# Kernel tuning notes

Hardware: AMD Instinct MI355X
Metric: run time of the kernel (lower is better)

## Reference

```python
import jax, jax.numpy as jnp
import numpy as np

# LeViT AttentionSubsample (use_conv=False), BatchNorm folded in eval mode (running stats).
B, RES, STRIDE, RES_OUT = 512, 14, 2, 7
N, NQ = RES * RES, RES_OUT * RES_OUT          # 196, 49
C, H, KD, VD = 256, 8, 16, 32                 # in_dim, heads, key_dim, val_dim
KV_DIM, Q_DIM, V_ATTN, OUT_DIM = H * (KD + VD), H * KD, H * VD, 384
EPS = 1e-5
SCALE = KD ** -0.5


def _bias_idxs():
    ii, jj = np.meshgrid(np.arange(RES), np.arange(RES), indexing='ij')
    k_pos = np.stack([ii.ravel(), jj.ravel()])                      # [2, 196]
    qi, qj = np.meshgrid(np.arange(0, RES, STRIDE), np.arange(0, RES, STRIDE), indexing='ij')
    q_pos = np.stack([qi.ravel(), qj.ravel()])                      # [2, 49]
    rel = np.abs(q_pos[:, :, None] - k_pos[:, None, :])             # [2, 49, 196]
    return jnp.asarray(rel[0] * RES + rel[1], dtype=jnp.int32)      # [49, 196]


def setup_inputs() -> dict:
    key = jax.random.key(0)
    ks = jax.random.split(key, 8)
    f32 = jnp.float32
    inp = {
        'x': jax.random.normal(ks[0], (B, N, C), f32),
        # LinearNorm kv: Linear(C -> KV_DIM, no bias) + BN1d
        'W_kv': jax.random.normal(ks[1], (KV_DIM, C), f32) * 0.05,
        'g_kv': jnp.ones((KV_DIM,), f32), 'b_kv': jnp.zeros((KV_DIM,), f32),
        'm_kv': jax.random.normal(ks[2], (KV_DIM,), f32) * 0.02,
        'v_kv': jax.random.uniform(ks[3], (KV_DIM,), f32) + 0.5,
        # LinearNorm q (after subsample)
        'W_q': jax.random.normal(ks[4], (Q_DIM, C), f32) * 0.05,
        'g_q': jnp.ones((Q_DIM,), f32), 'b_q': jnp.zeros((Q_DIM,), f32),
        'm_q': jax.random.normal(ks[5], (Q_DIM,), f32) * 0.02,
        'v_q': jax.random.uniform(ks[5], (Q_DIM,), f32) + 0.5,
        # proj: hardswish + LinearNorm(V_ATTN -> OUT_DIM)
        'W_proj': jax.random.normal(ks[6], (OUT_DIM, V_ATTN), f32) * 0.05,
        'g_proj': jnp.ones((OUT_DIM,), f32), 'b_proj': jnp.zeros((OUT_DIM,), f32),
        'm_proj': jax.random.normal(ks[7], (OUT_DIM,), f32) * 0.02,
        'v_proj': jax.random.uniform(ks[7], (OUT_DIM,), f32) + 0.5,
        'attention_biases': jax.random.normal(ks[2], (H, N), f32) * 0.02,
        'bias_idxs': _bias_idxs(),
    }
    return inp


def _linear_norm(x, W, g, b, m, v):
    y = jnp.einsum('...i,oi->...o', x, W)
    return (y - m) * (g * jax.lax.rsqrt(v + EPS)) + b


def _hardswish(x):
    return x * jnp.clip(x + 3.0, 0.0, 6.0) * (1.0 / 6.0)


def reference(x, W_kv, g_kv, b_kv, m_kv, v_kv, W_q, g_q, b_q, m_q, v_q,
              W_proj, g_proj, b_proj, m_proj, v_proj, attention_biases, bias_idxs):
    Bx = x.shape[0]
    kv = _linear_norm(x, W_kv, g_kv, b_kv, m_kv, v_kv).reshape(Bx, N, H, KD + VD)
    k, v = kv[..., :KD], kv[..., KD:]                                # [B,N,H,KD],[B,N,H,VD]
    xq = x.reshape(Bx, RES, RES, C)[:, ::STRIDE, ::STRIDE].reshape(Bx, NQ, C)
    q = _linear_norm(xq, W_q, g_q, b_q, m_q, v_q).reshape(Bx, NQ, H, KD)
    bias = attention_biases[:, bias_idxs]                            # [H, NQ, N]
    attn = jnp.einsum('bqhd,bkhd->bhqk', q, k) * SCALE + bias        # [B,H,NQ,N]
    attn = jax.nn.softmax(attn, axis=-1)
    o = jnp.einsum('bhqk,bkhd->bqhd', attn, v).reshape(Bx, NQ, V_ATTN)
    return _linear_norm(_hardswish(o), W_proj, g_proj, b_proj, m_proj, v_proj)
```

## Files before the change

kernel.cpp:

```cpp
#include <hip/hip_runtime.h>


#define Bn   512
#define Nn   196
#define NQn  49
#define Cn   256
#define Hn   8

typedef float    float4v __attribute__((ext_vector_type(4)));
typedef _Float16 half8v  __attribute__((ext_vector_type(8)));
typedef _Float16 half4v  __attribute__((ext_vector_type(4)));

__global__ __launch_bounds__(256) void prep_kernel(
    const float* __restrict__ Wkv, const float* __restrict__ Wq,
    const float* __restrict__ Wp,
    const float* __restrict__ g_kv, const float* __restrict__ b_kv,
    const float* __restrict__ m_kv, const float* __restrict__ v_kv,
    const float* __restrict__ g_q,  const float* __restrict__ b_q,
    const float* __restrict__ m_q,  const float* __restrict__ v_q,
    const float* __restrict__ g_p,  const float* __restrict__ b_p,
    const float* __restrict__ m_p,  const float* __restrict__ v_p,
    const float* __restrict__ ab,   const int* __restrict__ idxs,
    _Float16* __restrict__ WkvF, _Float16* __restrict__ WqF,
    _Float16* __restrict__ WpF,
    float* __restrict__ kv_s, float* __restrict__ kv_sh,
    float* __restrict__ q_s,  float* __restrict__ q_sh,
    float* __restrict__ p_s,  float* __restrict__ p_sh,
    float* __restrict__ biasF)
{
  int i = blockIdx.x * 256 + threadIdx.x;
  if (i < 12288) {
    int lane = i & 63, kc = (i >> 6) & 7, tile = i >> 9;
    const float* src = Wkv + (size_t)(tile * 16 + (lane & 15)) * Cn + kc * 32 + (lane >> 4) * 8;
    half8v hv;
#pragma unroll
    for (int j = 0; j < 8; ++j) hv[j] = (_Float16)src[j];
    *reinterpret_cast<half8v*>(WkvF + (size_t)i * 8) = hv;
    return;
  }
  i -= 12288;
  if (i < 4096) {
    int lane = i & 63, kc = (i >> 6) & 7, tile = i >> 9;
    const float* src = Wq + (size_t)(tile * 16 + (lane & 15)) * Cn + kc * 32 + (lane >> 4) * 8;
    half8v hv;
#pragma unroll
    for (int j = 0; j < 8; ++j) hv[j] = (_Float16)src[j];
    *reinterpret_cast<half8v*>(WqF + (size_t)i * 8) = hv;
    return;
  }
  i -= 4096;
  if (i < 12288) {
    int lane = i & 63, kc = (i >> 6) & 7, tile = i >> 9;
    const float* src = Wp + (size_t)(tile * 16 + (lane & 15)) * Cn + kc * 32 + (lane >> 4) * 8;
    half8v hv;
#pragma unroll
    for (int j = 0; j < 8; ++j) hv[j] = (_Float16)src[j];
    *reinterpret_cast<half8v*>(WpF + (size_t)i * 8) = hv;
    return;
  }
  i -= 12288;
  if (i < 26624) {
    int lane = i & 63;
    int v = i >> 6;
    int nt = v % 13;  v /= 13;
    int qt = v & 3, h = v >> 2;
    int r = lane & 15, g = lane >> 4;
    int n = nt * 16 + r; if (n > 195) n = 195;
    float4v bv;
#pragma unroll
    for (int j = 0; j < 4; ++j) {
      int q = qt * 16 + g * 4 + j; if (q > 48) q = 48;
      bv[j] = ab[h * Nn + idxs[q * Nn + n]];
    }
    *reinterpret_cast<float4v*>(biasF + (size_t)i * 4) = bv;
    return;
  }
  i -= 26624;
  if (i < 896) {
    if (i < 384) {
      float s = g_kv[i] * rsqrtf(v_kv[i] + 1e-5f);
      kv_s[i] = s; kv_sh[i] = b_kv[i] - m_kv[i] * s;
    } else if (i < 512) {
      int j = i - 384;
      float s = g_q[j] * rsqrtf(v_q[j] + 1e-5f);
      q_s[j] = 0.25f * s; q_sh[j] = 0.25f * (b_q[j] - m_q[j] * s);
    } else {
      int j = i - 512;
      float s = g_p[j] * rsqrtf(v_p[j] + 1e-5f);
      p_s[j] = s; p_sh[j] = b_p[j] - m_p[j] * s;
    }
  }
}

__global__ __launch_bounds__(512) void kv_gemm_kernel(
    const float* __restrict__ x, const _Float16* __restrict__ WkvF,
    const float* __restrict__ kv_s, const float* __restrict__ kv_sh,
    _Float16* __restrict__ kkF, _Float16* __restrict__ vF)
{
  const int b = blockIdx.x;
  const int by = blockIdx.y;
  const int ts = (by == 0) ? 0 : (3 * by + 1);
  const int cnt = (by == 0) ? 4 : 3;
  const int tid = threadIdx.x, lane = tid & 63, wid = tid >> 6;
  const int cg = lane >> 4, ci = lane & 15;

  __shared__ _Float16 sxf[4 * 8 * 64 * 8];

#pragma unroll
  for (int r = 0; r < 4; ++r) {
    int c = r * 512 + tid;
    int ln = c & 63, kc = (c >> 6) & 7, tl = c >> 9;
    int m = ln & 15, g = ln >> 4;
    int t = (ts + tl) * 16 + m;
    half8v hv;
    if (t < Nn) {
      const float* src = x + ((size_t)b * Nn + t) * Cn + kc * 32 + g * 8;
      float4v a0 = *reinterpret_cast<const float4v*>(src);
      float4v a1 = *reinterpret_cast<const float4v*>(src + 4);
      hv[0]=(_Float16)a0[0]; hv[1]=(_Float16)a0[1]; hv[2]=(_Float16)a0[2]; hv[3]=(_Float16)a0[3];
      hv[4]=(_Float16)a1[0]; hv[5]=(_Float16)a1[1]; hv[6]=(_Float16)a1[2]; hv[7]=(_Float16)a1[3];
    } else {
      hv = (half8v)(_Float16)0.f;
    }
    *reinterpret_cast<half8v*>(sxf + (size_t)c * 8) = hv;
  }
  __syncthreads();

  const int h = wid;
  const _Float16* Wb = WkvF + (size_t)(3 * h) * 8 * 64 * 8;
  half8v wk[8], w0[8], w1[8];
#pragma unroll
  for (int kc = 0; kc < 8; ++kc) {
    wk[kc] = *reinterpret_cast<const half8v*>(Wb + (size_t)(kc * 64 + lane) * 8);
    w0[kc] = *reinterpret_cast<const half8v*>(Wb + (size_t)((8 + kc) * 64 + lane) * 8);
    w1[kc] = *reinterpret_cast<const half8v*>(Wb + (size_t)((16 + kc) * 64 + lane) * 8);
  }
  float sk[4], shk[4];
#pragma unroll
  for (int j = 0; j < 4; ++j) {
    sk[j]  = kv_s [48 * h + cg * 4 + j];
    shk[j] = kv_sh[48 * h + cg * 4 + j];
  }
  const float sv0 = kv_s[48 * h + 16 + ci], shv0 = kv_sh[48 * h + 16 + ci];
  const float sv1 = kv_s[48 * h + 32 + ci], shv1 = kv_sh[48 * h + 32 + ci];

  const size_t bh = (size_t)b * 8 + h;
  for (int tl = 0; tl < cnt; ++tl) {
    half8v af[8];
#pragma unroll
    for (int kc = 0; kc < 8; ++kc)
      af[kc] = *reinterpret_cast<const half8v*>(sxf + (size_t)((tl * 8 + kc) * 64 + lane) * 8);
    const int t16 = ts + tl;
    float4v a0 = (float4v){0.f,0.f,0.f,0.f};
    float4v a1 = (float4v){0.f,0.f,0.f,0.f};
    float4v a2 = (float4v){0.f,0.f,0.f,0.f};
#pragma unroll
    for (int kc = 0; kc < 8; ++kc) {
      a0 = __builtin_amdgcn_mfma_f32_16x16x32_f16(wk[kc], af[kc], a0, 0, 0, 0);
      a1 = __builtin_amdgcn_mfma_f32_16x16x32_f16(af[kc], w0[kc], a1, 0, 0, 0);
      a2 = __builtin_amdgcn_mfma_f32_16x16x32_f16(af[kc], w1[kc], a2, 0, 0, 0);
    }
    half4v hk, h0, h1;
#pragma unroll
    for (int j = 0; j < 4; ++j) {
      hk[j] = (_Float16)(a0[j] * sk[j] + shk[j]);
      h0[j] = (_Float16)(a1[j] * sv0 + shv0);
      h1[j] = (_Float16)(a2[j] * sv1 + shv1);
    }
    *reinterpret_cast<half4v*>(kkF + ((bh * 13 + t16) * 64 + lane) * 4)           = hk;
    *reinterpret_cast<half4v*>(vF  + (((bh * 13 + t16) * 2 + 0) * 64 + lane) * 4) = h0;
    *reinterpret_cast<half4v*>(vF  + (((bh * 13 + t16) * 2 + 1) * 64 + lane) * 4) = h1;
  }
}

__global__ __launch_bounds__(256) void q_gemm_kernel(
    const float* __restrict__ x, const _Float16* __restrict__ WqF,
    const float* __restrict__ q_s, const float* __restrict__ q_sh,
    _Float16* __restrict__ qF)
{
  const int b = blockIdx.x, qt = blockIdx.y;
  const int tid = threadIdx.x, lane = tid & 63, wid = tid >> 6;
  const int cg = lane >> 4, mq = lane & 15;

  const int q = qt * 16 + mq;
  half8v af[8];
  if (q < NQn) {
    const int qi = q / 7, qj = q - qi * 7;
    const int tok = 28 * qi + 2 * qj;
    const float* src = x + ((size_t)b * Nn + tok) * Cn + cg * 8;
#pragma unroll
    for (int kc = 0; kc < 8; ++kc) {
      float4v a0 = *reinterpret_cast<const float4v*>(src + kc * 32);
      float4v a1 = *reinterpret_cast<const float4v*>(src + kc * 32 + 4);
      half8v t;
      t[0]=(_Float16)a0[0]; t[1]=(_Float16)a0[1]; t[2]=(_Float16)a0[2]; t[3]=(_Float16)a0[3];
      t[4]=(_Float16)a1[0]; t[5]=(_Float16)a1[1]; t[6]=(_Float16)a1[2]; t[7]=(_Float16)a1[3];
      af[kc] = t;
    }
  } else {
#pragma unroll
    for (int kc = 0; kc < 8; ++kc) af[kc] = (half8v)(_Float16)0.f;
  }

#pragma unroll
  for (int hh = 0; hh < 2; ++hh) {
    const int h = wid * 2 + hh;
    half8v wq[8];
#pragma unroll
    for (int kc = 0; kc < 8; ++kc)
      wq[kc] = *reinterpret_cast<const half8v*>(WqF + (size_t)((h * 8 + kc) * 64 + lane) * 8);
    float4v acc = (float4v){0.f,0.f,0.f,0.f};
#pragma unroll
    for (int kc = 0; kc < 8; ++kc)
      acc = __builtin_amdgcn_mfma_f32_16x16x32_f16(wq[kc], af[kc], acc, 0, 0, 0);
    half4v hq;
#pragma unroll
    for (int j = 0; j < 4; ++j) {
      int c = 16 * h + cg * 4 + j;
      hq[j] = (_Float16)(acc[j] * q_s[c] + q_sh[c]);
    }
    *reinterpret_cast<half4v*>(qF + ((((size_t)b * 8 + h) * 4 + qt) * 64 + lane) * 4) = hq;
  }
}

__global__ __launch_bounds__(256) void attn_kernel(
    const _Float16* __restrict__ kkF, const _Float16* __restrict__ vF,
    const _Float16* __restrict__ qF, const float* __restrict__ biasF,
    _Float16* __restrict__ oh)
{
  const int bh = blockIdx.x;
  const int b = bh >> 3, h = bh & 7;
  const int tid = threadIdx.x, lane = tid & 63, wid = tid >> 6;
  const int row_in = lane & 15, kgrp = lane >> 4;

  __shared__ _Float16 sP[4][16][212];

  half4v aq = *reinterpret_cast<const half4v*>(
      qF + (((size_t)bh * 4 + wid) * 64 + lane) * 4);
  const _Float16* kb = kkF + (size_t)bh * 13 * 64 * 4;
  const float* bb = biasF + (size_t)(h * 4 + wid) * 13 * 64 * 4;

  float4v acc[13];
#pragma unroll
  for (int nt = 0; nt < 13; ++nt) {
    half4v bk = *reinterpret_cast<const half4v*>(kb + (nt * 64 + lane) * 4);
    float4v a = (float4v){0.f,0.f,0.f,0.f};
    a = __builtin_amdgcn_mfma_f32_16x16x16f16(aq, bk, a, 0, 0, 0);
    float4v bias = *reinterpret_cast<const float4v*>(bb + (size_t)(nt * 64 + lane) * 4);
    acc[nt] = a + bias;
  }

  const bool tail_ok = (row_in < 4);
  float mx[4], sm[4];
#pragma unroll
  for (int i = 0; i < 4; ++i) mx[i] = -1e30f;
#pragma unroll
  for (int nt = 0; nt < 13; ++nt) {
    bool valid = (nt < 12) | tail_ok;
#pragma unroll
    for (int i = 0; i < 4; ++i)
      mx[i] = fmaxf(mx[i], valid ? acc[nt][i] : -1e30f);
  }
#pragma unroll
  for (int i = 0; i < 4; ++i) {
#pragma unroll
    for (int off = 8; off >= 1; off >>= 1)
      mx[i] = fmaxf(mx[i], __shfl_xor(mx[i], off, 64));
  }
#pragma unroll
  for (int i = 0; i < 4; ++i) sm[i] = 0.f;
#pragma unroll
  for (int nt = 0; nt < 13; ++nt) {
    bool valid = (nt < 12) | tail_ok;
#pragma unroll
    for (int i = 0; i < 4; ++i) {
      float e = valid ? __expf(acc[nt][i] - mx[i]) : 0.f;
      acc[nt][i] = e; sm[i] += e;
    }
  }
#pragma unroll
  for (int i = 0; i < 4; ++i) {
#pragma unroll
    for (int off = 8; off >= 1; off >>= 1)
      sm[i] += __shfl_xor(sm[i], off, 64);
  }
  float inv[4];
#pragma unroll
  for (int i = 0; i < 4; ++i) inv[i] = 1.f / sm[i];

#pragma unroll
  for (int nt = 0; nt < 13; ++nt)
#pragma unroll
    for (int i = 0; i < 4; ++i)
      sP[wid][kgrp * 4 + i][nt * 16 + row_in] = (_Float16)(acc[nt][i] * inv[i]);

  const _Float16* vb = vF + (size_t)bh * 13 * 2 * 64 * 4;
  float4v o0 = (float4v){0.f,0.f,0.f,0.f};
  float4v o1 = (float4v){0.f,0.f,0.f,0.f};
#pragma unroll
  for (int kc = 0; kc < 13; ++kc) {
    half4v ap  = *reinterpret_cast<const half4v*>(&sP[wid][row_in][kc * 16 + kgrp * 4]);
    half4v bv0 = *reinterpret_cast<const half4v*>(vb + ((kc * 2 + 0) * 64 + lane) * 4);
    half4v bv1 = *reinterpret_cast<const half4v*>(vb + ((kc * 2 + 1) * 64 + lane) * 4);
    o0 = __builtin_amdgcn_mfma_f32_16x16x16f16(ap, bv0, o0, 0, 0, 0);
    o1 = __builtin_amdgcn_mfma_f32_16x16x16f16(ap, bv1, o1, 0, 0, 0);
  }
#pragma unroll
  for (int i = 0; i < 4; ++i) {
    int q = wid * 16 + kgrp * 4 + i;
    if (q < NQn) {
      size_t base = ((size_t)b * NQn + q) * 256 + h * 32 + row_in;
      float v0 = o0[i], v1 = o1[i];
      float hs0 = v0 * fminf(fmaxf(v0 + 3.f, 0.f), 6.f) * (1.f / 6.f);
      float hs1 = v1 * fminf(fmaxf(v1 + 3.f, 0.f), 6.f) * (1.f / 6.f);
      oh[base]      = (_Float16)hs0;
      oh[base + 16] = (_Float16)hs1;
    }
  }
}

__global__ __launch_bounds__(256) void proj_kernel(
    const _Float16* __restrict__ oh, const _Float16* __restrict__ WpF,
    const float* __restrict__ p_s, const float* __restrict__ p_sh,
    float* __restrict__ out)
{
  const int tid = threadIdx.x, lane = tid & 63, wid = tid >> 6;
  const int row_in = lane & 15, kgrp = lane >> 4;
  const size_t g_a = (size_t)blockIdx.x * 64 + wid * 16 + row_in;
  const int jt0 = blockIdx.y * 8;

  half8v af[8];
  const _Float16* arow = oh + g_a * 256 + kgrp * 8;
#pragma unroll
  for (int kc = 0; kc < 8; ++kc)
    af[kc] = *reinterpret_cast<const half8v*>(arow + kc * 32);

  const size_t r0 = (size_t)blockIdx.x * 64 + wid * 16 + kgrp * 4;
#pragma unroll
  for (int nt = 0; nt < 8; ++nt) {
    float4v acc = (float4v){0.f,0.f,0.f,0.f};
#pragma unroll
    for (int kc = 0; kc < 8; ++kc) {
      half8v bf = *reinterpret_cast<const half8v*>(
          WpF + (size_t)(((jt0 + nt) * 8 + kc) * 64 + lane) * 8);
      acc = __builtin_amdgcn_mfma_f32_16x16x32_f16(af[kc], bf, acc, 0, 0, 0);
    }
    int j = (jt0 + nt) * 16 + row_in;
    float s = p_s[j], sh = p_sh[j];
#pragma unroll
    for (int i = 0; i < 4; ++i)
      out[(r0 + i) * 384 + j] = acc[i] * s + sh;
  }
}

extern "C" void kernel_launch(void* const* d_in, const int* in_sizes, int n_in,
                              void* d_out, int out_size, void* d_ws, size_t ws_size,
                              hipStream_t stream) {
  const float* x    = (const float*)d_in[0];
  const float* Wkv  = (const float*)d_in[1];
  const float* g_kv = (const float*)d_in[2];
  const float* b_kv = (const float*)d_in[3];
  const float* m_kv = (const float*)d_in[4];
  const float* v_kv = (const float*)d_in[5];
  const float* Wq   = (const float*)d_in[6];
  const float* g_q  = (const float*)d_in[7];
  const float* b_q  = (const float*)d_in[8];
  const float* m_q  = (const float*)d_in[9];
  const float* v_q  = (const float*)d_in[10];
  const float* Wp   = (const float*)d_in[11];
  const float* g_p  = (const float*)d_in[12];
  const float* b_p  = (const float*)d_in[13];
  const float* m_p  = (const float*)d_in[14];
  const float* v_p  = (const float*)d_in[15];
  const float* ab   = (const float*)d_in[16];
  const int*   idxs = (const int*)d_in[17];
  float* out = (float*)d_out;

  char* w = (char*)d_ws;
  _Float16* oh    = (_Float16*)(w);
  _Float16* kkF   = (_Float16*)(w + 12845056);
  _Float16* vF    = (_Float16*)(w + 40108032);
  _Float16* qF    = (_Float16*)(w + 94633984);
  _Float16* WkvF  = (_Float16*)(w + 103022592);
  _Float16* WqF   = (_Float16*)(w + 103219200);
  _Float16* WpF   = (_Float16*)(w + 103284736);
  float*    biasF = (float*)   (w + 103481344);
  float*    kv_s  = (float*)   (w + 103907328);
  float*    kv_sh = (float*)   (w + 103908864);
  float*    q_s   = (float*)   (w + 103910400);
  float*    q_sh  = (float*)   (w + 103910912);
  float*    p_s   = (float*)   (w + 103911424);
  float*    p_sh  = (float*)   (w + 103912960);

  prep_kernel<<<220, 256, 0, stream>>>(Wkv, Wq, Wp,
                                       g_kv, b_kv, m_kv, v_kv,
                                       g_q, b_q, m_q, v_q,
                                       g_p, b_p, m_p, v_p,
                                       ab, idxs,
                                       WkvF, WqF, WpF,
                                       kv_s, kv_sh, q_s, q_sh, p_s, p_sh, biasF);
  kv_gemm_kernel<<<dim3(Bn, 4), 512, 0, stream>>>(x, WkvF, kv_s, kv_sh, kkF, vF);
  q_gemm_kernel<<<dim3(Bn, 4), 256, 0, stream>>>(x, WqF, q_s, q_sh, qF);
  attn_kernel<<<Bn * Hn, 256, 0, stream>>>(kkF, vF, qF, biasF, oh);
  proj_kernel<<<dim3(392, 3), 256, 0, stream>>>(oh, WpF, p_s, p_sh, out);
}
```

Before: 292.9 us.

## Fuse q projection into kv GEMM kernel and restructure loops for weight reuse

The separate q_gemm kernel is merged into the kv GEMM kernel as a fifth grid slice along y, so one launch covers both projections. The loop order is inverted: weights are loaded once per k-chunk and applied to all four token tiles, with accumulators held across tiles instead of keeping all weights in registers. The q slice now stages the strided-subsampled x through shared memory, and launch bounds request 4 blocks per CU. The cost is more accumulator registers, and the kv path always computes four tiles even when only three are stored.

```diff
diff --git a/kernel.cpp b/kernel.cpp
--- a/kernel.cpp
+++ b/kernel.cpp
@@ -92,134 +92,142 @@
   }
 }
 
-__global__ __launch_bounds__(512) void kv_gemm_kernel(
-    const float* __restrict__ x, const _Float16* __restrict__ WkvF,
+__global__ __launch_bounds__(512, 4) void kvq_gemm_kernel(
+    const float* __restrict__ x,
+    const _Float16* __restrict__ WkvF, const _Float16* __restrict__ WqF,
     const float* __restrict__ kv_s, const float* __restrict__ kv_sh,
-    _Float16* __restrict__ kkF, _Float16* __restrict__ vF)
+    const float* __restrict__ q_s,  const float* __restrict__ q_sh,
+    _Float16* __restrict__ kkF, _Float16* __restrict__ vF,
+    _Float16* __restrict__ qF)
 {
-  const int b = blockIdx.x;
-  const int by = blockIdx.y;
-  const int ts = (by == 0) ? 0 : (3 * by + 1);
-  const int cnt = (by == 0) ? 4 : 3;
+  const int b = blockIdx.x, by = blockIdx.y;
   const int tid = threadIdx.x, lane = tid & 63, wid = tid >> 6;
   const int cg = lane >> 4, ci = lane & 15;
 
   __shared__ _Float16 sxf[4 * 8 * 64 * 8];
 
-#pragma unroll
-  for (int r = 0; r < 4; ++r) {
-    int c = r * 512 + tid;
-    int ln = c & 63, kc = (c >> 6) & 7, tl = c >> 9;
-    int m = ln & 15, g = ln >> 4;
-    int t = (ts + tl) * 16 + m;
-    half8v hv;
-    if (t < Nn) {
-      const float* src = x + ((size_t)b * Nn + t) * Cn + kc * 32 + g * 8;
-      float4v a0 = *reinterpret_cast<const float4v*>(src);
-      float4v a1 = *reinterpret_cast<const float4v*>(src + 4);
-      hv[0]=(_Float16)a0[0]; hv[1]=(_Float16)a0[1]; hv[2]=(_Float16)a0[2]; hv[3]=(_Float16)a0[3];
-      hv[4]=(_Float16)a1[0]; hv[5]=(_Float16)a1[1]; hv[6]=(_Float16)a1[2]; hv[7]=(_Float16)a1[3];
-    } else {
-      hv = (half8v)(_Float16)0.f;
-    }
-    *reinterpret_cast<half8v*>(sxf + (size_t)c * 8) = hv;
-  }
-  __syncthreads();
-
-  const int h = wid;
-  const _Float16* Wb = WkvF + (size_t)(3 * h) * 8 * 64 * 8;
-  half8v wk[8], w0[8], w1[8];
-#pragma unroll
-  for (int kc = 0; kc < 8; ++kc) {
-    wk[kc] = *reinterpret_cast<const half8v*>(Wb + (size_t)(kc * 64 + lane) * 8);
-    w0[kc] = *reinterpret_cast<const half8v*>(Wb + (size_t)((8 + kc) * 64 + lane) * 8);
-    w1[kc] = *reinterpret_cast<const half8v*>(Wb + (size_t)((16 + kc) * 64 + lane) * 8);
-  }
-  float sk[4], shk[4];
-#pragma unroll
-  for (int j = 0; j < 4; ++j) {
-    sk[j]  = kv_s [48 * h + cg * 4 + j];
-    shk[j] = kv_sh[48 * h + cg * 4 + j];
-  }
-  const float sv0 = kv_s[48 * h + 16 + ci], shv0 = kv_sh[48 * h + 16 + ci];
-  const float sv1 = kv_s[48 * h + 32 + ci], shv1 = kv_sh[48 * h + 32 + ci];
-
-  const size_t bh = (size_t)b * 8 + h;
-  for (int tl = 0; tl < cnt; ++tl) {
-    half8v af[8];
-#pragma unroll
-    for (int kc = 0; kc < 8; ++kc)
-      af[kc] = *reinterpret_cast<const half8v*>(sxf + (size_t)((tl * 8 + kc) * 64 + lane) * 8);
-    const int t16 = ts + tl;
-    float4v a0 = (float4v){0.f,0.f,0.f,0.f};
-    float4v a1 = (float4v){0.f,0.f,0.f,0.f};
-    float4v a2 = (float4v){0.f,0.f,0.f,0.f};
+  if (by < 4) {
+    const int ts = (by == 0) ? 0 : (3 * by + 1);
+    const int cnt = (by == 0) ? 4 : 3;
+
+#pragma unroll
+    for (int r = 0; r < 4; ++r) {
+      int c = r * 512 + tid;
+      int ln = c & 63, kc = (c >> 6) & 7, tl = c >> 9;
+      int t = (ts + tl) * 16 + (ln & 15);
+      half8v hv;
+      if (t < Nn) {
+        const float* src = x + ((size_t)b * Nn + t) * Cn + kc * 32 + (ln >> 4) * 8;
+        float4v a0 = *reinterpret_cast<const float4v*>(src);
+        float4v a1 = *reinterpret_cast<const float4v*>(src + 4);
+        hv[0]=(_Float16)a0[0]; hv[1]=(_Float16)a0[1]; hv[2]=(_Float16)a0[2]; hv[3]=(_Float16)a0[3];
+        hv[4]=(_Float16)a1[0]; hv[5]=(_Float16)a1[1]; hv[6]=(_Float16)a1[2]; hv[7]=(_Float16)a1[3];
+      } else {
+        hv = (half8v)(_Float16)0.f;
+      }
+      *reinterpret_cast<half8v*>(sxf + (size_t)c * 8) = hv;
+    }
+    __syncthreads();
+
+    const int h = wid;
+    const _Float16* Wb = WkvF + (size_t)(3 * h) * 8 * 64 * 8;
+
+    float4v acK[4], acV0[4], acV1[4];
+#pragma unroll
+    for (int tl = 0; tl < 4; ++tl) {
+      acK[tl]  = (float4v){0.f,0.f,0.f,0.f};
+      acV0[tl] = (float4v){0.f,0.f,0.f,0.f};
+      acV1[tl] = (float4v){0.f,0.f,0.f,0.f};
+    }
 #pragma unroll
     for (int kc = 0; kc < 8; ++kc) {
-      a0 = __builtin_amdgcn_mfma_f32_16x16x32_f16(wk[kc], af[kc], a0, 0, 0, 0);
-      a1 = __builtin_amdgcn_mfma_f32_16x16x32_f16(af[kc], w0[kc], a1, 0, 0, 0);
-      a2 = __builtin_amdgcn_mfma_f32_16x16x32_f16(af[kc], w1[kc], a2, 0, 0, 0);
-    }
-    half4v hk, h0, h1;
+      half8v wk = *reinterpret_cast<const half8v*>(Wb + (size_t)(kc * 64 + lane) * 8);
+      half8v w0 = *reinterpret_cast<const half8v*>(Wb + (size_t)((8 + kc) * 64 + lane) * 8);
+      half8v w1 = *reinterpret_cast<const half8v*>(Wb + (size_t)((16 + kc) * 64 + lane) * 8);
+#pragma unroll
+      for (int tl = 0; tl < 4; ++tl) {
+        half8v a = *reinterpret_cast<const half8v*>(sxf + (size_t)((tl * 8 + kc) * 64 + lane) * 8);
+        acK[tl]  = __builtin_amdgcn_mfma_f32_16x16x32_f16(wk, a, acK[tl], 0, 0, 0);
+        acV0[tl] = __builtin_amdgcn_mfma_f32_16x16x32_f16(a, w0, acV0[tl], 0, 0, 0);
+        acV1[tl] = __builtin_amdgcn_mfma_f32_16x16x32_f16(a, w1, acV1[tl], 0, 0, 0);
+      }
+    }
+
+    float sk0[4], shk0[4];
 #pragma unroll
     for (int j = 0; j < 4; ++j) {
-      hk[j] = (_Float16)(a0[j] * sk[j] + shk[j]);
-      h0[j] = (_Float16)(a1[j] * sv0 + shv0);
-      h1[j] = (_Float16)(a2[j] * sv1 + shv1);
-    }
-    *reinterpret_cast<half4v*>(kkF + ((bh * 13 + t16) * 64 + lane) * 4)           = hk;
-    *reinterpret_cast<half4v*>(vF  + (((bh * 13 + t16) * 2 + 0) * 64 + lane) * 4) = h0;
-    *reinterpret_cast<half4v*>(vF  + (((bh * 13 + t16) * 2 + 1) * 64 + lane) * 4) = h1;
-  }
-}
-
-__global__ __launch_bounds__(256) void q_gemm_kernel(
-    const float* __restrict__ x, const _Float16* __restrict__ WqF,
-    const float* __restrict__ q_s, const float* __restrict__ q_sh,
-    _Float16* __restrict__ qF)
-{
-  const int b = blockIdx.x, qt = blockIdx.y;
-  const int tid = threadIdx.x, lane = tid & 63, wid = tid >> 6;
-  const int cg = lane >> 4, mq = lane & 15;
-
-  const int q = qt * 16 + mq;
-  half8v af[8];
-  if (q < NQn) {
-    const int qi = q / 7, qj = q - qi * 7;
-    const int tok = 28 * qi + 2 * qj;
-    const float* src = x + ((size_t)b * Nn + tok) * Cn + cg * 8;
+      sk0[j]  = kv_s [48 * h + cg * 4 + j];
+      shk0[j] = kv_sh[48 * h + cg * 4 + j];
+    }
+    const float sv0 = kv_s[48 * h + 16 + ci], shv0 = kv_sh[48 * h + 16 + ci];
+    const float sv1 = kv_s[48 * h + 32 + ci], shv1 = kv_sh[48 * h + 32 + ci];
+    const size_t bh = (size_t)b * 8 + h;
+
+#pragma unroll
+    for (int tl = 0; tl < 4; ++tl) {
+      if (tl < cnt) {
+        const int t16 = ts + tl;
+        half4v hk, h0, h1;
+#pragma unroll
+        for (int j = 0; j < 4; ++j) {
+          hk[j] = (_Float16)(acK[tl][j]  * sk0[j] + shk0[j]);
+          h0[j] = (_Float16)(acV0[tl][j] * sv0 + shv0);
+          h1[j] = (_Float16)(acV1[tl][j] * sv1 + shv1);
+        }
+        *reinterpret_cast<half4v*>(kkF + ((bh * 13 + t16) * 64 + lane) * 4)           = hk;
+        *reinterpret_cast<half4v*>(vF  + (((bh * 13 + t16) * 2 + 0) * 64 + lane) * 4) = h0;
+        *reinterpret_cast<half4v*>(vF  + (((bh * 13 + t16) * 2 + 1) * 64 + lane) * 4) = h1;
+      }
+    }
+  } else {
+#pragma unroll
+    for (int r = 0; r < 4; ++r) {
+      int c = r * 512 + tid;
+      int ln = c & 63, kc = (c >> 6) & 7, tl = c >> 9;
+      int qi_ = tl * 16 + (ln & 15);
+      half8v hv;
+      if (qi_ < NQn) {
+        int qr = qi_ / 7, qc2 = qi_ - qr * 7;
+        int t = 28 * qr + 2 * qc2;
+        const float* src = x + ((size_t)b * Nn + t) * Cn + kc * 32 + (ln >> 4) * 8;
+        float4v a0 = *reinterpret_cast<const float4v*>(src);
+        float4v a1 = *reinterpret_cast<const float4v*>(src + 4);
+        hv[0]=(_Float16)a0[0]; hv[1]=(_Float16)a0[1]; hv[2]=(_Float16)a0[2]; hv[3]=(_Float16)a0[3];
+        hv[4]=(_Float16)a1[0]; hv[5]=(_Float16)a1[1]; hv[6]=(_Float16)a1[2]; hv[7]=(_Float16)a1[3];
+      } else {
+        hv = (half8v)(_Float16)0.f;
+      }
+      *reinterpret_cast<half8v*>(sxf + (size_t)c * 8) = hv;
+    }
+    __syncthreads();
+
+    const int h = wid;
+    float4v acQ[4];
+#pragma unroll
+    for (int tl = 0; tl < 4; ++tl) acQ[tl] = (float4v){0.f,0.f,0.f,0.f};
 #pragma unroll
     for (int kc = 0; kc < 8; ++kc) {
-      float4v a0 = *reinterpret_cast<const float4v*>(src + kc * 32);
-      float4v a1 = *reinterpret_cast<const float4v*>(src + kc * 32 + 4);
-      half8v t;
-      t[0]=(_Float16)a0[0]; t[1]=(_Float16)a0[1]; t[2]=(_Float16)a0[2]; t[3]=(_Float16)a0[3];
-      t[4]=(_Float16)a1[0]; t[5]=(_Float16)a1[1]; t[6]=(_Float16)a1[2]; t[7]=(_Float16)a1[3];
-      af[kc] = t;
-    }
-  } else {
-#pragma unroll
-    for (int kc = 0; kc < 8; ++kc) af[kc] = (half8v)(_Float16)0.f;
-  }
-
-#pragma unroll
-  for (int hh = 0; hh < 2; ++hh) {
-    const int h = wid * 2 + hh;
-    half8v wq[8];
-#pragma unroll
-    for (int kc = 0; kc < 8; ++kc)
-      wq[kc] = *reinterpret_cast<const half8v*>(WqF + (size_t)((h * 8 + kc) * 64 + lane) * 8);
-    float4v acc = (float4v){0.f,0.f,0.f,0.f};
-#pragma unroll
-    for (int kc = 0; kc < 8; ++kc)
-      acc = __builtin_amdgcn_mfma_f32_16x16x32_f16(wq[kc], af[kc], acc, 0, 0, 0);
-    half4v hq;
+      half8v wq = *reinterpret_cast<const half8v*>(WqF + (size_t)((h * 8 + kc) * 64 + lane) * 8);
+#pragma unroll
+      for (int tl = 0; tl < 4; ++tl) {
+        half8v a = *reinterpret_cast<const half8v*>(sxf + (size_t)((tl * 8 + kc) * 64 + lane) * 8);
+        acQ[tl] = __builtin_amdgcn_mfma_f32_16x16x32_f16(wq, a, acQ[tl], 0, 0, 0);
+      }
+    }
+    float sq_[4], shq_[4];
 #pragma unroll
     for (int j = 0; j < 4; ++j) {
       int c = 16 * h + cg * 4 + j;
-      hq[j] = (_Float16)(acc[j] * q_s[c] + q_sh[c]);
-    }
-    *reinterpret_cast<half4v*>(qF + ((((size_t)b * 8 + h) * 4 + qt) * 64 + lane) * 4) = hq;
+      sq_[j] = q_s[c]; shq_[j] = q_sh[c];
+    }
+#pragma unroll
+    for (int tl = 0; tl < 4; ++tl) {
+      half4v hq;
+#pragma unroll
+      for (int j = 0; j < 4; ++j)
+        hq[j] = (_Float16)(acQ[tl][j] * sq_[j] + shq_[j]);
+      *reinterpret_cast<half4v*>(qF + ((((size_t)b * 8 + h) * 4 + tl) * 64 + lane) * 4) = hq;
+    }
   }
 }
 
@@ -399,8 +407,9 @@
                                        ab, idxs,
                                        WkvF, WqF, WpF,
                                        kv_s, kv_sh, q_s, q_sh, p_s, p_sh, biasF);
-  kv_gemm_kernel<<<dim3(Bn, 4), 512, 0, stream>>>(x, WkvF, kv_s, kv_sh, kkF, vF);
-  q_gemm_kernel<<<dim3(Bn, 4), 256, 0, stream>>>(x, WqF, q_s, q_sh, qF);
+  kvq_gemm_kernel<<<dim3(Bn, 5), 512, 0, stream>>>(x, WkvF, WqF,
+                                                   kv_s, kv_sh, q_s, q_sh,
+                                                   kkF, vF, qF);
   attn_kernel<<<Bn * Hn, 256, 0, stream>>>(kkF, vF, qF, biasF, oh);
   proj_kernel<<<dim3(392, 3), 256, 0, stream>>>(oh, WpF, p_s, p_sh, out);
 }
```

After: 282.7 us. 3.5% less time.
